# Optimization experiments

Measured on AMD Instinct MI355X. Metric: run time of the kernel, lower is better.

The kernel has to match this reference:

```python
import jax, jax.numpy as jnp
import numpy as np

HEADS = 8
DIM_HEAD = 64
DIM = 512
SCALE = DIM_HEAD ** -0.5
BN_EPS = 1e-5


def setup_inputs() -> dict:
    key = jax.random.key(0)
    ks = jax.random.split(key, 5)
    b, p = 8, 2048
    init = 0.05
    return {
        "x": jax.random.normal(ks[0], (b, p, DIM), jnp.float32),
        "wq": jax.random.normal(ks[1], (HEADS, DIM_HEAD, DIM // HEADS), jnp.float32) * init,
        "wk": jax.random.normal(ks[2], (HEADS, DIM_HEAD, DIM // HEADS), jnp.float32) * init,
        "wv": jax.random.normal(ks[3], (HEADS, DIM_HEAD, DIM // HEADS), jnp.float32) * init,
        "wo": jax.random.normal(ks[4], (DIM, HEADS * DIM_HEAD), jnp.float32) * init,
        "gamma": jnp.ones((DIM,), jnp.float32),
        "beta": jnp.zeros((DIM,), jnp.float32),
    }


def reference(x, wq, wk, wv, wo, gamma, beta):
    # x: [b, p, d]
    b, p, d = x.shape
    h, e = HEADS, DIM_HEAD
    # grouped 1x1 conv == per-head linear on the head's channel slice
    xg = x.reshape(b, p, h, d // h)            # [b, p, h, c]
    q = jnp.einsum('bphc,hec->bhpe', xg, wq)   # [b, h, p, e]
    k = jnp.einsum('bphc,hec->bhpe', xg, wk)
    v = jnp.einsum('bphc,hec->bhpe', xg, wv)
    dots = jnp.einsum('bhie,bhje->bhij', q, k) * SCALE
    attn = jax.nn.softmax(dots, axis=-1)
    out = jnp.einsum('bhij,bhje->bhie', attn, v)     # [b, h, p, e]
    out = out.transpose(0, 2, 1, 3).reshape(b, p, h * e)  # [b, p, inner]
    out = jnp.einsum('bpi,di->bpd', out, wo)         # output 1x1 conv, no bias
    # BatchNorm1d (training mode): stats over (batch, points) per channel
    mean = out.mean(axis=(0, 1))
    var = out.var(axis=(0, 1))
    out = (out - mean) * jax.lax.rsqrt(var + BN_EPS) * gamma + beta
    return jax.nn.relu(out)                          # [b, p, d]
```

## Files before the change

kernel.cpp:

```cpp
#include <hip/hip_runtime.h>
#include <hip/hip_bf16.h>

#define B_ 8
#define P_ 2048
#define D_ 512
#define H_ 8
#define N_ (B_*P_)

using f32x4  = __attribute__((ext_vector_type(4))) float;
using f32x16 = __attribute__((ext_vector_type(16))) float;
using bf16x8 = __attribute__((ext_vector_type(8))) short;

__device__ __forceinline__ unsigned f2bf2(float lo, float hi){
    unsigned short a = __bfloat16_as_ushort(__float2bfloat16(lo));
    unsigned short b = __bfloat16_as_ushort(__float2bfloat16(hi));
    return (unsigned)a | ((unsigned)b << 16);
}
__device__ __forceinline__ unsigned short f2bfu(float x){
    return __bfloat16_as_ushort(__float2bfloat16(x));
}
__device__ __forceinline__ float bf2f(unsigned short u){
    return __uint_as_float(((unsigned)u) << 16);
}
#define SW(r, cb) ((cb) ^ (((r) & 7) << 4))

__device__ __forceinline__ bf16x8 lds_frag(const unsigned char* base, int row, int colb){
    return *(const bf16x8*)(base + row*128 + SW(row, colb));
}

#if __has_builtin(__builtin_amdgcn_exp2f)
#define EXP2(x) __builtin_amdgcn_exp2f(x)
#else
#define EXP2(x) exp2f(x)
#endif

__device__ __forceinline__ void plane32_swap(unsigned &a, unsigned &b){
#if __has_builtin(__builtin_amdgcn_permlane32_swap)
    auto r = __builtin_amdgcn_permlane32_swap(a, b, false, false);
    a = r[0]; b = r[1];
#else
    asm volatile("s_nop 1\n\tv_permlane32_swap_b32 %0, %1\n\ts_nop 1"
                 : "+v"(a), "+v"(b));
#endif
}

#define QSCALE 0.18033688011112042f

__device__ __forceinline__ size_t kf_off(int bh, int tt, int kb, int ec, int hi, int l32){
    return ((size_t)(bh*32 + tt))*4096 + (size_t)(((((kb*4 + ec)*2 + hi)*32) + l32)*8);
}
__device__ __forceinline__ size_t vf_off(int bh, int tt, int ks, int eb, int hi, int l32){
    return ((size_t)(bh*32 + tt))*4096 + (size_t)(((((ks*2 + eb)*2 + hi)*32) + l32)*8);
}

__global__ __launch_bounds__(256) void qkv_proj(
        const float* __restrict__ x,
        const float* __restrict__ wq, const float* __restrict__ wk, const float* __restrict__ wv,
        unsigned short* __restrict__ Q, unsigned short* __restrict__ Kf, unsigned short* __restrict__ Vf)
{
    __shared__ unsigned char xs[128*128];
    __shared__ unsigned char wsh[3][64*128];
    const int t  = threadIdx.x;
    const int bh = blockIdx.x, b = bh >> 3, h = bh & 7;
    const int p0 = blockIdx.y * 128;

    {
        int r = t >> 1, half = t & 1;
        const float4* src = (const float4*)(x + (size_t)(b*P_ + p0 + r)*D_ + h*64 + half*32);
        #pragma unroll
        for (int ci = 0; ci < 4; ci++){
            float4 a = src[ci*2], c = src[ci*2+1];
            uint4 w;
            w.x = f2bf2(a.x, a.y); w.y = f2bf2(a.z, a.w);
            w.z = f2bf2(c.x, c.y); w.w = f2bf2(c.z, c.w);
            *(uint4*)(xs + r*128 + SW(r, half*64 + ci*16)) = w;
        }
    }
    if (t < 192){
        int m = t >> 6, r = t & 63;
        const float* wp = (m == 0 ? wq : (m == 1 ? wk : wv));
        const float4* src = (const float4*)(wp + (size_t)(h*64 + r)*64);
        float sc = (m == 0) ? QSCALE : 1.0f;
        #pragma unroll
        for (int ci = 0; ci < 8; ci++){
            float4 a = src[ci*2], c = src[ci*2+1];
            a.x*=sc;a.y*=sc;a.z*=sc;a.w*=sc; c.x*=sc;c.y*=sc;c.z*=sc;c.w*=sc;
            uint4 w;
            w.x = f2bf2(a.x, a.y); w.y = f2bf2(a.z, a.w);
            w.z = f2bf2(c.x, c.y); w.w = f2bf2(c.z, c.w);
            *(uint4*)(wsh[m] + r*128 + SW(r, ci*16)) = w;
        }
    }
    __syncthreads();
    const int wid = t >> 6, lane = t & 63, g = lane >> 4, l16 = lane & 15;

    bf16x8 fx[2][2];
    #pragma unroll
    for (int pt = 0; pt < 2; pt++)
        #pragma unroll
        for (int kk = 0; kk < 2; kk++)
            fx[pt][kk] = lds_frag(xs, wid*32 + pt*16 + l16, kk*64 + 16*g);

    #pragma unroll
    for (int m = 0; m < 2; m++){
        #pragma unroll
        for (int et = 0; et < 4; et++){
            bf16x8 fw0 = lds_frag(wsh[m], et*16 + l16, 16*g);
            bf16x8 fw1 = lds_frag(wsh[m], et*16 + l16, 64 + 16*g);
            #pragma unroll
            for (int pt = 0; pt < 2; pt++){
                f32x4 acc = {0.f,0.f,0.f,0.f};
                acc = __builtin_amdgcn_mfma_f32_16x16x32_bf16(fw0, fx[pt][0], acc, 0,0,0);
                acc = __builtin_amdgcn_mfma_f32_16x16x32_bf16(fw1, fx[pt][1], acc, 0,0,0);
                int p  = p0 + wid*32 + pt*16 + l16;
                int e0 = et*16 + 4*g;
                uint2 w2; w2.x = f2bf2(acc[0], acc[1]); w2.y = f2bf2(acc[2], acc[3]);
                if (m == 0){
                    *(uint2*)(Q + (size_t)(bh*P_ + p)*64 + e0) = w2;
                } else {
                    int tt = p >> 6, kvr = p & 63;
                    *(uint2*)(Kf + kf_off(bh, tt, kvr >> 5, et, g >> 1, kvr & 31) + 4*(g & 1)) = w2;
                }
            }
        }
    }
    #pragma unroll
    for (int et = 0; et < 4; et++){
        bf16x8 fw0 = lds_frag(wsh[2], et*16 + l16, 16*g);
        bf16x8 fw1 = lds_frag(wsh[2], et*16 + l16, 64 + 16*g);
        #pragma unroll
        for (int pt = 0; pt < 2; pt++){
            f32x4 acc = {0.f,0.f,0.f,0.f};
            acc = __builtin_amdgcn_mfma_f32_16x16x32_bf16(fx[pt][0], fw0, acc, 0,0,0);
            acc = __builtin_amdgcn_mfma_f32_16x16x32_bf16(fx[pt][1], fw1, acc, 0,0,0);
            int e  = et*16 + l16;
            int pb = p0 + wid*32 + pt*16 + 4*g;
            int tt = pb >> 6, kvc = pb & 63;
            uint2 w2; w2.x = f2bf2(acc[0], acc[1]); w2.y = f2bf2(acc[2], acc[3]);
            *(uint2*)(Vf + vf_off(bh, tt, kvc >> 4, e >> 5, (kvc >> 3) & 1, e & 31) + (kvc & 7)) = w2;
        }
    }
}

__global__ __launch_bounds__(256, 2) void attn_fwd(
        const unsigned short* __restrict__ Q, const unsigned short* __restrict__ Kf,
        const unsigned short* __restrict__ Vf, unsigned short* __restrict__ AO)
{
    const int t  = threadIdx.x;
    const int id = blockIdx.x;
    const int vix = (id & 7) * 64 + (id >> 3);
    const int bh = vix >> 3, b = bh >> 3, h = bh & 7;
    const int q0 = (vix & 7) * 256;
    const int lane = t & 63, wid = t >> 6, hi = lane >> 5, l32 = lane & 31;

    const int qa = q0 + wid*64 + l32;

    bf16x8 fq[2][4];
    #pragma unroll
    for (int qs = 0; qs < 2; qs++)
        #pragma unroll
        for (int ec = 0; ec < 4; ec++)
            fq[qs][ec] = *(const bf16x8*)(Q + (size_t)(bh*P_ + qa + qs*32)*64 + ec*16 + hi*8);

    const unsigned short* kfp = Kf + kf_off(bh, 0, 0, 0, hi, l32);
    const unsigned short* vfp = Vf + vf_off(bh, 0, 0, 0, hi, l32);

    f32x16 aco[2][2];
    #pragma unroll
    for (int r = 0; r < 16; r++){
        aco[0][0][r] = 0.f; aco[0][1][r] = 0.f;
        aco[1][0][r] = 0.f; aco[1][1][r] = 0.f;
    }
    float sml[2] = {0.f, 0.f};

    #pragma unroll 1
    for (int tt = 0; tt < 32; tt++){
        const unsigned short* kp = kfp + (size_t)tt * 4096;
        const unsigned short* vp = vfp + (size_t)tt * 4096;
        __builtin_amdgcn_s_setprio(1);
        #pragma unroll
        for (int kb = 0; kb < 2; kb++){
            bf16x8 fk[4], fv[4];
            #pragma unroll
            for (int ec = 0; ec < 4; ec++)
                fk[ec] = *(const bf16x8*)(kp + kb*2048 + ec*512);
            #pragma unroll
            for (int sg = 0; sg < 2; sg++)
                #pragma unroll
                for (int eb = 0; eb < 2; eb++)
                    fv[sg*2+eb] = *(const bf16x8*)(vp + (kb*2+sg)*1024 + eb*512);

            #pragma unroll
            for (int qs = 0; qs < 2; qs++){
                f32x16 s;
                #pragma unroll
                for (int r = 0; r < 16; r++) s[r] = 0.f;
                #pragma unroll
                for (int ec = 0; ec < 4; ec++)
                    s = __builtin_amdgcn_mfma_f32_32x32x16_bf16(fk[ec], fq[qs][ec], s, 0, 0, 0);
                float p[16];
                float rs = 0.f;
                #pragma unroll
                for (int r = 0; r < 16; r++){ p[r] = EXP2(s[r]); rs += p[r]; }
                sml[qs] += rs;
                #pragma unroll
                for (int sg = 0; sg < 2; sg++){
                    unsigned A0 = f2bf2(p[sg*8+0], p[sg*8+1]);
                    unsigned A1 = f2bf2(p[sg*8+2], p[sg*8+3]);
                    unsigned A2 = f2bf2(p[sg*8+4], p[sg*8+5]);
                    unsigned A3 = f2bf2(p[sg*8+6], p[sg*8+7]);
                    plane32_swap(A0, A2);
                    plane32_swap(A1, A3);
                    union { unsigned u[4]; bf16x8 v; } pfu;
                    pfu.u[0] = A0; pfu.u[1] = A1; pfu.u[2] = A2; pfu.u[3] = A3;
                    #pragma unroll
                    for (int eb = 0; eb < 2; eb++)
                        aco[qs][eb] = __builtin_amdgcn_mfma_f32_32x32x16_bf16(fv[sg*2+eb], pfu.v, aco[qs][eb], 0, 0, 0);
                }
            }
        }
        __builtin_amdgcn_s_setprio(0);
    }

    #pragma unroll
    for (int qs = 0; qs < 2; qs++){
        float l = sml[qs] + __shfl_xor(sml[qs], 32);
        float inv = 1.f / l;
        unsigned short* aor = AO + (size_t)(b*P_ + qa + qs*32)*D_ + h*64;
        #pragma unroll
        for (int eb = 0; eb < 2; eb++)
            #pragma unroll
            for (int rq = 0; rq < 4; rq++){
                uint2 w;
                w.x = f2bf2(aco[qs][eb][rq*4+0]*inv, aco[qs][eb][rq*4+1]*inv);
                w.y = f2bf2(aco[qs][eb][rq*4+2]*inv, aco[qs][eb][rq*4+3]*inv);
                *(uint2*)(aor + eb*32 + rq*8 + hi*4) = w;
            }
    }
}

__global__ __launch_bounds__(256) void wo_gemm(
        const unsigned short* __restrict__ AO, const float* __restrict__ wo,
        unsigned short* __restrict__ ao2, float* __restrict__ sums)
{
    __shared__ unsigned char ash[128*128];
    __shared__ unsigned char wsh[64*128];
    __shared__ float red[4][2][64];
    const int t  = threadIdx.x;
    const int d0 = blockIdx.x * 64;
    const int n0 = blockIdx.y * 128;
    const int wid = t >> 6, lane = t & 63, g = lane >> 4, l16 = lane & 15;

    f32x4 acc[2][4];
    #pragma unroll
    for (int mt = 0; mt < 2; mt++)
        #pragma unroll
        for (int dt = 0; dt < 4; dt++) acc[mt][dt] = (f32x4){0.f,0.f,0.f,0.f};

    for (int kc = 0; kc < 8; kc++){
        __syncthreads();
        {
            int r = t >> 1, half = t & 1;
            const uint4* src = (const uint4*)(AO + (size_t)(n0 + r)*D_ + kc*64 + half*32);
            #pragma unroll
            for (int i = 0; i < 4; i++)
                *(uint4*)(ash + r*128 + SW(r, half*64 + i*16)) = src[i];
        }
        if (t < 128){
            int r = t >> 1, half = t & 1;
            const float4* src = (const float4*)(wo + (size_t)(d0 + r)*D_ + kc*64 + half*32);
            #pragma unroll
            for (int ci = 0; ci < 4; ci++){
                float4 a = src[ci*2], c = src[ci*2+1];
                uint4 w;
                w.x = f2bf2(a.x, a.y); w.y = f2bf2(a.z, a.w);
                w.z = f2bf2(c.x, c.y); w.w = f2bf2(c.z, c.w);
                *(uint4*)(wsh + r*128 + SW(r, half*64 + ci*16)) = w;
            }
        }
        __syncthreads();
        #pragma unroll
        for (int kk = 0; kk < 2; kk++){
            bf16x8 fa[2], fw[4];
            #pragma unroll
            for (int mt = 0; mt < 2; mt++) fa[mt] = lds_frag(ash, wid*32 + mt*16 + l16, kk*64 + 16*g);
            #pragma unroll
            for (int dt = 0; dt < 4; dt++) fw[dt] = lds_frag(wsh, dt*16 + l16, kk*64 + 16*g);
            #pragma unroll
            for (int mt = 0; mt < 2; mt++)
                #pragma unroll
                for (int dt = 0; dt < 4; dt++)
                    acc[mt][dt] = __builtin_amdgcn_mfma_f32_16x16x32_bf16(fa[mt], fw[dt], acc[mt][dt], 0,0,0);
        }
    }
    float s1[4] = {0.f,0.f,0.f,0.f}, s2[4] = {0.f,0.f,0.f,0.f};
    #pragma unroll
    for (int mt = 0; mt < 2; mt++)
        #pragma unroll
        for (int dt = 0; dt < 4; dt++){
            int d = d0 + dt*16 + l16;
            #pragma unroll
            for (int r = 0; r < 4; r++){
                float v = acc[mt][dt][r];
                ao2[(size_t)(n0 + wid*32 + mt*16 + 4*g + r)*D_ + d] = f2bfu(v);
                s1[dt] += v; s2[dt] += v*v;
            }
        }
    #pragma unroll
    for (int dt = 0; dt < 4; dt++){
        s1[dt] += __shfl_xor(s1[dt], 16); s1[dt] += __shfl_xor(s1[dt], 32);
        s2[dt] += __shfl_xor(s2[dt], 16); s2[dt] += __shfl_xor(s2[dt], 32);
    }
    if (g == 0){
        #pragma unroll
        for (int dt = 0; dt < 4; dt++){
            red[wid][0][dt*16 + l16] = s1[dt];
            red[wid][1][dt*16 + l16] = s2[dt];
        }
    }
    __syncthreads();
    if (t < 128){
        int which = t >> 6, ch = t & 63;
        float v = red[0][which][ch] + red[1][which][ch] + red[2][which][ch] + red[3][which][ch];
        atomicAdd(&sums[which*D_ + d0 + ch], v);
    }
}

__global__ void bn_zero(float* sums){ sums[threadIdx.x] = 0.f; }

__global__ void bn_stats(const float* __restrict__ sums, const float* __restrict__ gamma,
                         const float* __restrict__ beta, float* __restrict__ coef)
{
    int d = threadIdx.x;
    float mean = sums[d] * (1.f/16384.f);
    float var  = sums[512 + d] * (1.f/16384.f) - mean*mean;
    float sc   = gamma[d] * rsqrtf(var + 1e-5f);
    coef[d]       = sc;
    coef[512 + d] = beta[d] - mean*sc;
}

__global__ __launch_bounds__(256) void bn_apply(const unsigned short* __restrict__ ao2,
                                                float* __restrict__ out, const float* __restrict__ coef)
{
    __shared__ float cs[1024];
    int t = threadIdx.x;
    #pragma unroll
    for (int i = 0; i < 4; i++) cs[t + i*256] = coef[t + i*256];
    __syncthreads();
    const int total = N_ * D_ / 8;
    for (int idx = blockIdx.x*256 + t; idx < total; idx += gridDim.x*256){
        uint4 v = *(const uint4*)(ao2 + (size_t)idx*8);
        int d = (idx & 63) * 8;
        float4 o0, o1;
        o0.x = fmaxf(0.f, bf2f((unsigned short)(v.x      ))*cs[d+0] + cs[512+d+0]);
        o0.y = fmaxf(0.f, bf2f((unsigned short)(v.x >> 16))*cs[d+1] + cs[512+d+1]);
        o0.z = fmaxf(0.f, bf2f((unsigned short)(v.y      ))*cs[d+2] + cs[512+d+2]);
        o0.w = fmaxf(0.f, bf2f((unsigned short)(v.y >> 16))*cs[d+3] + cs[512+d+3]);
        o1.x = fmaxf(0.f, bf2f((unsigned short)(v.z      ))*cs[d+4] + cs[512+d+4]);
        o1.y = fmaxf(0.f, bf2f((unsigned short)(v.z >> 16))*cs[d+5] + cs[512+d+5]);
        o1.z = fmaxf(0.f, bf2f((unsigned short)(v.w      ))*cs[d+6] + cs[512+d+6]);
        o1.w = fmaxf(0.f, bf2f((unsigned short)(v.w >> 16))*cs[d+7] + cs[512+d+7]);
        *(float4*)(out + (size_t)idx*8)     = o0;
        *(float4*)(out + (size_t)idx*8 + 4) = o1;
    }
}

extern "C" void kernel_launch(void* const* d_in, const int* in_sizes, int n_in,
                              void* d_out, int out_size, void* d_ws, size_t ws_size,
                              hipStream_t stream)
{
    const float* x     = (const float*)d_in[0];
    const float* wq    = (const float*)d_in[1];
    const float* wk    = (const float*)d_in[2];
    const float* wv    = (const float*)d_in[3];
    const float* wo    = (const float*)d_in[4];
    const float* gamma = (const float*)d_in[5];
    const float* beta  = (const float*)d_in[6];
    float* out = (float*)d_out;

    unsigned char* ws = (unsigned char*)d_ws;
    unsigned short* Q  = (unsigned short*)(ws);
    unsigned short* Kf = (unsigned short*)(ws + (16u<<20));
    unsigned short* Vf = (unsigned short*)(ws + (32u<<20));
    unsigned short* AO = (unsigned short*)(ws + (48u<<20));
    float* sums = (float*)(ws + (64u<<20));
    float* coef = sums + 1024;
    unsigned short* AO2 = Q;

    hipLaunchKernelGGL(bn_zero,  dim3(1),       dim3(1024), 0, stream, sums);
    hipLaunchKernelGGL(qkv_proj, dim3(64, 16),  dim3(256),  0, stream, x, wq, wk, wv, Q, Kf, Vf);
    hipLaunchKernelGGL(attn_fwd, dim3(512),     dim3(256),  0, stream, Q, Kf, Vf, AO);
    hipLaunchKernelGGL(wo_gemm,  dim3(8, 128),  dim3(256),  0, stream, AO, wo, AO2, sums);
    hipLaunchKernelGGL(bn_stats, dim3(1),       dim3(512),  0, stream, sums, gamma, beta, coef);
    hipLaunchKernelGGL(bn_apply, dim3(2048),    dim3(256),  0, stream, AO2, out, coef);
}
```

Before: 162.6 us.

## Split KV range across two wave groups in attention and combine via LDS

Doubles the attention block to 512 threads, with the second group of four waves handling the second half of the KV tiles for the same queries. Each group runs half the loop iterations. The second group's partial accumulators and row sums are written to shared memory, and the first group adds them in before normalising and storing. The aim is more waves in flight per CU to hide memory latency. The costs are a large LDS exchange buffer, an extra barrier, and a tighter register budget per thread under the new launch bounds, which could cause spills.

```diff
diff --git a/kernel.cpp b/kernel.cpp
--- a/kernel.cpp
+++ b/kernel.cpp
@@ -142,18 +142,20 @@
     }
 }
 
-__global__ __launch_bounds__(256, 2) void attn_fwd(
+__global__ __launch_bounds__(512, 2) void attn_fwd(
         const unsigned short* __restrict__ Q, const unsigned short* __restrict__ Kf,
         const unsigned short* __restrict__ Vf, unsigned short* __restrict__ AO)
 {
+    __shared__ float xch[4][64][69];
     const int t  = threadIdx.x;
     const int id = blockIdx.x;
     const int vix = (id & 7) * 64 + (id >> 3);
     const int bh = vix >> 3, b = bh >> 3, h = bh & 7;
     const int q0 = (vix & 7) * 256;
     const int lane = t & 63, wid = t >> 6, hi = lane >> 5, l32 = lane & 31;
-
-    const int qa = q0 + wid*64 + l32;
+    const int qw = wid & 3, sp = wid >> 2;
+
+    const int qa = q0 + qw*64 + l32;
 
     bf16x8 fq[2][4];
     #pragma unroll
@@ -162,8 +164,8 @@
         for (int ec = 0; ec < 4; ec++)
             fq[qs][ec] = *(const bf16x8*)(Q + (size_t)(bh*P_ + qa + qs*32)*64 + ec*16 + hi*8);
 
-    const unsigned short* kfp = Kf + kf_off(bh, 0, 0, 0, hi, l32);
-    const unsigned short* vfp = Vf + vf_off(bh, 0, 0, 0, hi, l32);
+    const unsigned short* kfp = Kf + kf_off(bh, sp*16, 0, 0, hi, l32);
+    const unsigned short* vfp = Vf + vf_off(bh, sp*16, 0, 0, hi, l32);
 
     f32x16 aco[2][2];
     #pragma unroll
@@ -174,7 +176,7 @@
     float sml[2] = {0.f, 0.f};
 
     #pragma unroll 1
-    for (int tt = 0; tt < 32; tt++){
+    for (int tt = 0; tt < 16; tt++){
         const unsigned short* kp = kfp + (size_t)tt * 4096;
         const unsigned short* vp = vfp + (size_t)tt * 4096;
         __builtin_amdgcn_s_setprio(1);
@@ -222,20 +224,46 @@
         __builtin_amdgcn_s_setprio(0);
     }
 
-    #pragma unroll
-    for (int qs = 0; qs < 2; qs++){
-        float l = sml[qs] + __shfl_xor(sml[qs], 32);
-        float inv = 1.f / l;
-        unsigned short* aor = AO + (size_t)(b*P_ + qa + qs*32)*D_ + h*64;
-        #pragma unroll
-        for (int eb = 0; eb < 2; eb++)
-            #pragma unroll
-            for (int rq = 0; rq < 4; rq++){
-                uint2 w;
-                w.x = f2bf2(aco[qs][eb][rq*4+0]*inv, aco[qs][eb][rq*4+1]*inv);
-                w.y = f2bf2(aco[qs][eb][rq*4+2]*inv, aco[qs][eb][rq*4+3]*inv);
-                *(uint2*)(aor + eb*32 + rq*8 + hi*4) = w;
-            }
+    if (sp == 1){
+        float* dst = xch[qw][lane];
+        #pragma unroll
+        for (int qs = 0; qs < 2; qs++)
+            #pragma unroll
+            for (int eb = 0; eb < 2; eb++)
+                #pragma unroll
+                for (int r = 0; r < 16; r++)
+                    dst[(qs*2 + eb)*16 + r] = aco[qs][eb][r];
+        dst[64] = sml[0];
+        dst[65] = sml[1];
+    }
+    __syncthreads();
+    if (sp == 0){
+        const float* src = xch[qw][lane];
+        #pragma unroll
+        for (int qs = 0; qs < 2; qs++)
+            #pragma unroll
+            for (int eb = 0; eb < 2; eb++)
+                #pragma unroll
+                for (int r = 0; r < 16; r++)
+                    aco[qs][eb][r] += src[(qs*2 + eb)*16 + r];
+        sml[0] += src[64];
+        sml[1] += src[65];
+
+        #pragma unroll
+        for (int qs = 0; qs < 2; qs++){
+            float l = sml[qs] + __shfl_xor(sml[qs], 32);
+            float inv = 1.f / l;
+            unsigned short* aor = AO + (size_t)(b*P_ + qa + qs*32)*D_ + h*64;
+            #pragma unroll
+            for (int eb = 0; eb < 2; eb++)
+                #pragma unroll
+                for (int rq = 0; rq < 4; rq++){
+                    uint2 w;
+                    w.x = f2bf2(aco[qs][eb][rq*4+0]*inv, aco[qs][eb][rq*4+1]*inv);
+                    w.y = f2bf2(aco[qs][eb][rq*4+2]*inv, aco[qs][eb][rq*4+3]*inv);
+                    *(uint2*)(aor + eb*32 + rq*8 + hi*4) = w;
+                }
+        }
     }
 }
 
@@ -389,7 +417,7 @@
 
     hipLaunchKernelGGL(bn_zero,  dim3(1),       dim3(1024), 0, stream, sums);
     hipLaunchKernelGGL(qkv_proj, dim3(64, 16),  dim3(256),  0, stream, x, wq, wk, wv, Q, Kf, Vf);
-    hipLaunchKernelGGL(attn_fwd, dim3(512),     dim3(256),  0, stream, Q, Kf, Vf, AO);
+    hipLaunchKernelGGL(attn_fwd, dim3(512),     dim3(512),  0, stream, Q, Kf, Vf, AO);
     hipLaunchKernelGGL(wo_gemm,  dim3(8, 128),  dim3(256),  0, stream, AO, wo, AO2, sums);
     hipLaunchKernelGGL(bn_stats, dim3(1),       dim3(512),  0, stream, sums, gamma, beta, coef);
     hipLaunchKernelGGL(bn_apply, dim3(2048),    dim3(256),  0, stream, AO2, out, coef);
```

New measurement: 176.0 us. 1.08x slower.
